# Performance work log

Measured on AMD Instinct MI355X. Metric: run time of the kernel, lower is better.

The kernel has to match this reference:

```python
import jax, jax.numpy as jnp
import numpy as np
import math

NUM_HEADS = 4
HIDDEN = 256
HEAD_DIM = HIDDEN // NUM_HEADS
NEG = jnp.finfo(jnp.float32).min


def setup_inputs() -> dict:
    key = jax.random.key(0)
    ks = jax.random.split(key, 8)
    B, Q, K = 4, 2048, 2048
    q_hidden_states = jax.random.normal(ks[0], (B, Q, HIDDEN), dtype=jnp.float32)
    k_hidden_states = jax.random.normal(ks[1], (B, K, HIDDEN), dtype=jnp.float32)
    attention_mask = jnp.zeros((B, 1, Q, K), dtype=jnp.float32)
    align_mask = jax.random.randint(ks[2], (B, K, Q), 0, 2, dtype=jnp.int32)
    s = 1.0 / math.sqrt(HIDDEN)
    Wq = jax.random.normal(ks[3], (HIDDEN, HIDDEN), dtype=jnp.float32) * s
    Wk = jax.random.normal(ks[4], (HIDDEN, HIDDEN), dtype=jnp.float32) * s
    Wv = jax.random.normal(ks[5], (HIDDEN, HIDDEN), dtype=jnp.float32) * s
    Wo = jax.random.normal(ks[6], (HIDDEN, HIDDEN), dtype=jnp.float32) * s
    return {"q_hidden_states": q_hidden_states, "k_hidden_states": k_hidden_states,
            "attention_mask": attention_mask, "align_mask": align_mask,
            "Wq": Wq, "Wk": Wk, "Wv": Wv, "Wo": Wo}


def reference(q_hidden_states, k_hidden_states, attention_mask, align_mask, Wq, Wk, Wv, Wo):
    B, Q, _ = q_hidden_states.shape
    K = k_hidden_states.shape[1]
    # torch Linear: y = x @ W.T  -> [B, S, H, D]
    q = (q_hidden_states @ Wq.T).reshape(B, Q, NUM_HEADS, HEAD_DIM)
    k = (k_hidden_states @ Wk.T).reshape(B, K, NUM_HEADS, HEAD_DIM)
    v = (k_hidden_states @ Wv.T).reshape(B, K, NUM_HEADS, HEAD_DIM)
    # scores: [B, H, Q, K]
    scores = jnp.einsum('bqhd,bkhd->bhqk', q, k) / math.sqrt(HEAD_DIM)
    # additive mask + clamp to finfo min
    scores = jnp.maximum(scores + attention_mask, NEG)
    # align_mask: (B, K, Q) -> (B, 1, Q, K); masked_fill where == 0
    am = jnp.transpose(align_mask, (0, 2, 1))[:, None, :, :]
    scores = jnp.where(am == 0, NEG, scores)
    scores = jnp.maximum(scores, NEG)
    probs = jax.nn.softmax(scores.astype(jnp.float32), axis=-1).astype(q.dtype)
    attn = jnp.einsum('bhqk,bkhd->bqhd', probs, v).reshape(B, Q, HIDDEN)
    return attn @ Wo.T
```

## Files before the change

### kernel.cpp

```cpp
#include <hip/hip_runtime.h>

#define NEGF -3.402823466e38f
#define MASKED_F -3.38953139e38f
#define LOG2E 1.44269504088896f
#define DEFER_THR 8.0f

typedef __attribute__((ext_vector_type(8))) short bf16x8;
typedef __attribute__((ext_vector_type(4))) float f32x4;
typedef __attribute__((ext_vector_type(4))) unsigned short u16x4;
typedef __attribute__((ext_vector_type(2))) unsigned int u32x2;

__device__ __forceinline__ unsigned short f2bf(float f) {
  unsigned u = __builtin_bit_cast(unsigned, f);
  u += 0x7fffu + ((u >> 16) & 1u);
  return (unsigned short)(u >> 16);
}

#define GLOAD_LDS16(gsrc, ldst)                                                     \
  __builtin_amdgcn_global_load_lds(                                                 \
      (const __attribute__((address_space(1))) void*)(gsrc),                        \
      (__attribute__((address_space(3))) void*)(ldst), 16, 0, 0)

#define OFF_QH  0u
#define OFF_KH  2097152u
#define OFF_W   4194304u
#define OFF_QP  4456448u
#define OFF_KP  6553600u
#define OFF_VT  8650752u
#define OFF_ATT 10747904u
#define OFF_M   12845056u
#define USHORT_USED 29622272u

__global__ __launch_bounds__(256) void k_convert(
    const float* __restrict__ qh, const float* __restrict__ kh,
    const float* __restrict__ w0, const float* __restrict__ w1,
    const float* __restrict__ w2, const float* __restrict__ w3,
    unsigned short* __restrict__ dst) {
  int v = blockIdx.x * 256 + threadIdx.x;
  const float* src;
  if (v < 524288)       src = qh + (size_t)v * 4;
  else if (v < 1048576) src = kh + ((size_t)v - 524288) * 4;
  else {
    int t = v - 1048576;
    int which = t >> 14;
    const float* w = (which == 0) ? w0 : (which == 1) ? w1 : (which == 2) ? w2 : w3;
    src = w + (size_t)(t & 16383) * 4;
  }
  f32x4 x = *(const f32x4*)src;
  u16x4 o;
  o[0] = f2bf(x[0]); o[1] = f2bf(x[1]); o[2] = f2bf(x[2]); o[3] = f2bf(x[3]);
  *(u16x4*)(dst + (size_t)v * 4) = o;
}

__global__ __launch_bounds__(256) void k_maskprep(const float* __restrict__ am,
    const int* __restrict__ al, unsigned short* __restrict__ M) {
  __shared__ float L[64 * 65];
  int bid = blockIdx.x;
  int b = bid >> 10, q64 = (bid >> 5) & 31, k64 = bid & 31;
  int t = threadIdx.x, c = t & 63, rg = t >> 6;

  const float* amb = am + ((size_t)b * 2048 + q64 * 64) * 2048 + k64 * 64;
#pragma unroll
  for (int i = 0; i < 16; ++i) {
    int row = i * 4 + rg;
    L[row * 65 + c] = amb[(size_t)row * 2048 + c] * LOG2E;
  }
  __syncthreads();
  const int* alb = al + ((size_t)b * 2048 + k64 * 64) * 2048 + q64 * 64;
#pragma unroll
  for (int i = 0; i < 16; ++i) {
    int kr = i * 4 + rg;
    if (alb[(size_t)kr * 2048 + c] == 0) L[c * 65 + kr] = MASKED_F;
  }
  __syncthreads();
  int w = t >> 6, lane = t & 63, l15 = lane & 15, l4 = lane >> 4;
  unsigned short* outp = M + ((((size_t)(b * 128 + q64 * 4 + w)) * 32 + k64) * 64 + lane) * 16;
#pragma unroll
  for (int kt = 0; kt < 4; ++kt) {
    u16x4 o;
#pragma unroll
    for (int r = 0; r < 4; ++r)
      o[r] = f2bf(L[(w * 16 + l15) * 65 + kt * 16 + l4 * 4 + r]);
    *(u16x4*)(outp + kt * 4) = o;
  }
}

__global__ __launch_bounds__(256) void k_proj(unsigned short* __restrict__ ws) {
  int bid = blockIdx.x;
  int mat = bid / 512;
  int rem = bid - mat * 512;
  int mt = rem >> 2, nt = rem & 3;
  int tid = threadIdx.x, w = tid >> 6, lane = tid & 63;
  int l15 = lane & 15, l4 = lane >> 4;

  const unsigned short* X = ws + (mat == 0 ? OFF_QH : OFF_KH);
  const unsigned short* W = ws + OFF_W + (size_t)mat * 65536;

  int i0 = mt * 64 + w * 16;
  int arow = i0 + l15;
  int koff = l4 * 8;

  f32x4 acc[4] = {};
  for (int ks = 0; ks < 8; ++ks) {
    bf16x8 a = *(const bf16x8*)(X + (size_t)arow * 256 + ks * 32 + koff);
#pragma unroll
    for (int ct = 0; ct < 4; ++ct) {
      bf16x8 bb = *(const bf16x8*)(W + (size_t)(nt * 64 + ct * 16 + l15) * 256 + ks * 32 + koff);
      acc[ct] = __builtin_amdgcn_mfma_f32_16x16x32_bf16(a, bb, acc[ct], 0, 0, 0);
    }
  }

  unsigned short* Qp = ws + OFF_QP;
  unsigned short* Kp = ws + OFF_KP;
  unsigned short* Vt = ws + OFF_VT;
  int rbase = i0 + l4 * 4;
#pragma unroll
  for (int ct = 0; ct < 4; ++ct) {
#pragma unroll
    for (int r = 0; r < 4; ++r) {
      int row = rbase + r;
      int b = row >> 11, s = row & 2047;
      int d = ct * 16 + l15;
      float v = acc[ct][r];
      if (mat == 0)      Qp[((size_t)(b * 4 + nt) * 2048 + s) * 64 + d] = f2bf(v * (0.125f * LOG2E));
      else if (mat == 1) Kp[((size_t)(b * 4 + nt) * 2048 + s) * 64 + d] = f2bf(v);
      else               Vt[((size_t)(b * 4 + nt) * 64 + d) * 2048 + s] = f2bf(v);
    }
  }
}

template <int NS>
__global__ __launch_bounds__(256) void k_attn(unsigned short* __restrict__ ws,
    float* __restrict__ po, float* __restrict__ pm, float* __restrict__ pl) {
  constexpr int LOG = (NS == 4) ? 2 : (NS == 2) ? 1 : 0;
  constexpr int SPAN = 2048 / NS;

  __shared__ __align__(16) unsigned short Kb[2][4096];
  __shared__ __align__(16) unsigned short Vb[2][4096];
  __shared__ __align__(16) unsigned short plds[4][1024];

  int bid = blockIdx.x;
  int sp = bid & (NS - 1);
  int qt = (bid >> LOG) & 31;
  int bh = bid >> (LOG + 5);
  int b = bh >> 2, h = bh & 3;
  int tid = threadIdx.x, w = tid >> 6, lane = tid & 63;
  int l15 = lane & 15, l4 = lane >> 4;
  int q0 = qt * 64 + w * 16;

  const unsigned short* Qp = ws + OFF_QP;
  const unsigned short* Kp = ws + OFF_KP + (size_t)bh * 2048 * 64;
  const unsigned short* Vt = ws + OFF_VT + (size_t)bh * 64 * 2048;
  const unsigned short* Mw = ws + OFF_M +
      (((size_t)(b * 128 + qt * 4 + w)) * 32) * 1024 + (size_t)lane * 16;

  int srow = lane >> 3;
  int scol = ((lane & 7) ^ srow) * 8;
  int c0 = w * 2;

  bf16x8 qf0 = *(const bf16x8*)(Qp + ((size_t)bh * 2048 + q0 + l15) * 64 + l4 * 8);
  bf16x8 qf1 = *(const bf16x8*)(Qp + ((size_t)bh * 2048 + q0 + l15) * 64 + 32 + l4 * 8);

  f32x4 o[4] = {};
  float mrun = -__builtin_inff();
  float lpart = 0.f;

  int kk0 = sp * SPAN;
#pragma unroll
  for (int c2 = 0; c2 < 2; ++c2) {
    int c = c0 + c2;
    GLOAD_LDS16(Kp + (size_t)(kk0 + c * 8 + srow) * 64 + scol, &Kb[0][c * 512]);
    GLOAD_LDS16(Vt + (size_t)(c * 8 + srow) * 2048 + kk0 + scol, &Vb[0][c * 512]);
  }
  __syncthreads();

  int cur = 0;
  for (int kk = kk0; kk < kk0 + SPAN; kk += 64) {
    if (kk + 64 < kk0 + SPAN) {
#pragma unroll
      for (int c2 = 0; c2 < 2; ++c2) {
        int c = c0 + c2;
        GLOAD_LDS16(Kp + (size_t)(kk + 64 + c * 8 + srow) * 64 + scol, &Kb[cur ^ 1][c * 512]);
        GLOAD_LDS16(Vt + (size_t)(c * 8 + srow) * 2048 + (kk + 64) + scol, &Vb[cur ^ 1][c * 512]);
      }
    }
    const unsigned short* mp = Mw + ((size_t)(kk >> 6)) * 1024;
    bf16x8 m0 = *(const bf16x8*)mp;
    bf16x8 m1 = *(const bf16x8*)(mp + 8);

    f32x4 sfr[4];
    __builtin_amdgcn_s_setprio(1);
#pragma unroll
    for (int kt = 0; kt < 4; ++kt) {
      int row = kt * 16 + l15;
      int sw = l15 & 7;
      bf16x8 k0 = *(const bf16x8*)&Kb[cur][row * 64 + ((l4 ^ sw) * 8)];
      bf16x8 k1 = *(const bf16x8*)&Kb[cur][row * 64 + (((4 + l4) ^ sw) * 8)];
      f32x4 acc = {};
      acc = __builtin_amdgcn_mfma_f32_16x16x32_bf16(k0, qf0, acc, 0, 0, 0);
      acc = __builtin_amdgcn_mfma_f32_16x16x32_bf16(k1, qf1, acc, 0, 0, 0);
      sfr[kt] = acc;
    }
    __builtin_amdgcn_s_setprio(0);

#pragma unroll
    for (int kt = 0; kt < 4; ++kt)
#pragma unroll
      for (int r = 0; r < 4; ++r) {
        int j = kt * 4 + r;
        unsigned short mu = (unsigned short)(j < 8 ? m0[j] : m1[j & 7]);
        sfr[kt][r] += __builtin_bit_cast(float, (unsigned)mu << 16);
      }

    float pmax = sfr[0][0];
#pragma unroll
    for (int kt = 0; kt < 4; ++kt)
#pragma unroll
      for (int r = 0; r < 4; ++r) pmax = fmaxf(pmax, sfr[kt][r]);
    pmax = fmaxf(pmax, __shfl_xor(pmax, 16));
    pmax = fmaxf(pmax, __shfl_xor(pmax, 32));

    if (__any(pmax > mrun + DEFER_THR)) {
      float mnew = fmaxf(mrun, pmax);
      float sfac = exp2f(mrun - mnew);
      mrun = mnew;
      lpart *= sfac;
#pragma unroll
      for (int r = 0; r < 4; ++r) {
        float sf = __shfl(sfac, l4 * 4 + r);
        o[0][r] *= sf; o[1][r] *= sf; o[2][r] *= sf; o[3][r] *= sf;
      }
    }

    float ls = 0.f;
#pragma unroll
    for (int kt = 0; kt < 4; ++kt)
#pragma unroll
      for (int r = 0; r < 4; ++r) {
        float e = exp2f(sfr[kt][r] - mrun);
        sfr[kt][r] = e;
        ls += e;
      }
    lpart += ls;

#pragma unroll
    for (int kt = 0; kt < 4; ++kt) {
      unsigned lo, hi;
      asm("v_cvt_pk_bf16_f32 %0, %1, %2" : "=v"(lo) : "v"(sfr[kt][0]), "v"(sfr[kt][1]));
      asm("v_cvt_pk_bf16_f32 %0, %1, %2" : "=v"(hi) : "v"(sfr[kt][2]), "v"(sfr[kt][3]));
      int chunk = kt * 2 + (l4 >> 1);
      int addr = l15 * 64 + (((chunk) ^ (l15 & 7)) << 3) + ((l4 & 1) << 2);
      u32x2 pk; pk[0] = lo; pk[1] = hi;
      *(u32x2*)&plds[w][addr] = pk;
    }

    __builtin_amdgcn_s_setprio(1);
#pragma unroll
    for (int ks = 0; ks < 2; ++ks) {
      int chnk = ks * 4 + l4;
      bf16x8 pa = *(const bf16x8*)&plds[w][l15 * 64 + ((chnk ^ (l15 & 7)) << 3)];
#pragma unroll
      for (int dt = 0; dt < 4; ++dt) {
        int row = dt * 16 + l15;
        bf16x8 vf = *(const bf16x8*)&Vb[cur][row * 64 + (((ks * 4 + l4) ^ (l15 & 7)) * 8)];
        o[dt] = __builtin_amdgcn_mfma_f32_16x16x32_bf16(pa, vf, o[dt], 0, 0, 0);
      }
    }
    __builtin_amdgcn_s_setprio(0);

    __syncthreads();
    cur ^= 1;
  }

  float lsum = lpart;
  lsum += __shfl_xor(lsum, 16);
  lsum += __shfl_xor(lsum, 32);

  if constexpr (NS == 1) {
    unsigned short* attnb = ws + OFF_ATT;
#pragma unroll
    for (int r = 0; r < 4; ++r) {
      float inv = 1.0f / __shfl(lsum, l4 * 4 + r);
      int qrow = q0 + l4 * 4 + r;
#pragma unroll
      for (int dt = 0; dt < 4; ++dt)
        attnb[(size_t)(b * 2048 + qrow) * 256 + h * 64 + dt * 16 + l15] = f2bf(o[dt][r] * inv);
    }
  } else {
    float* pob = po + (((size_t)sp * 16 + bh) * 2048) * 64;
#pragma unroll
    for (int r = 0; r < 4; ++r) {
      int qrow = q0 + l4 * 4 + r;
#pragma unroll
      for (int dt = 0; dt < 4; ++dt)
        pob[(size_t)qrow * 64 + dt * 16 + l15] = o[dt][r];
    }
    if (l4 == 0) {
      pm[(size_t)sp * 32768 + bh * 2048 + q0 + l15] = mrun;
      pl[(size_t)sp * 32768 + bh * 2048 + q0 + l15] = lsum;
    }
  }
}

template <int NS>
__global__ __launch_bounds__(256) void k_combine(const float* __restrict__ po,
    const float* __restrict__ pm, const float* __restrict__ pl,
    unsigned short* __restrict__ attnb) {
  int t = blockIdx.x * 256 + threadIdx.x;
  int d = t & 63;
  int row = t >> 6;

  float m[NS], l[NS];
  float M = -__builtin_inff();
#pragma unroll
  for (int sp = 0; sp < NS; ++sp) {
    m[sp] = pm[(size_t)sp * 32768 + row];
    l[sp] = pl[(size_t)sp * 32768 + row];
    M = fmaxf(M, m[sp]);
  }
  float denom = 0.f, acc = 0.f;
#pragma unroll
  for (int sp = 0; sp < NS; ++sp) {
    float wgt = exp2f(m[sp] - M);
    denom += l[sp] * wgt;
    acc += po[((size_t)sp * 32768 + row) * 64 + d] * wgt;
  }
  float val = acc / denom;
  int bh = row >> 11, qrow = row & 2047;
  int b = bh >> 2, h = bh & 3;
  attnb[((size_t)(b * 2048 + qrow)) * 256 + h * 64 + d] = f2bf(val);
}

__global__ __launch_bounds__(256) void k_oproj(const unsigned short* __restrict__ ws,
                                               float* __restrict__ out) {
  int bid = blockIdx.x;
  int mt = bid >> 2, nt = bid & 3;
  int tid = threadIdx.x, w = tid >> 6, lane = tid & 63;
  int l15 = lane & 15, l4 = lane >> 4;

  const unsigned short* A = ws + OFF_ATT;
  const unsigned short* W = ws + OFF_W + 3u * 65536u;
  int i0 = mt * 64 + w * 16;

  f32x4 acc[4] = {};
  for (int ks = 0; ks < 8; ++ks) {
    bf16x8 a = *(const bf16x8*)(A + (size_t)(i0 + l15) * 256 + ks * 32 + l4 * 8);
#pragma unroll
    for (int ct = 0; ct < 4; ++ct) {
      bf16x8 bb = *(const bf16x8*)(W + (size_t)(nt * 64 + ct * 16 + l15) * 256 + ks * 32 + l4 * 8);
      acc[ct] = __builtin_amdgcn_mfma_f32_16x16x32_bf16(a, bb, acc[ct], 0, 0, 0);
    }
  }
#pragma unroll
  for (int ct = 0; ct < 4; ++ct)
#pragma unroll
    for (int r = 0; r < 4; ++r)
      out[(size_t)(i0 + l4 * 4 + r) * 256 + nt * 64 + ct * 16 + l15] = acc[ct][r];
}

extern "C" void kernel_launch(void* const* d_in, const int* in_sizes, int n_in,
                              void* d_out, int out_size, void* d_ws, size_t ws_size,
                              hipStream_t stream) {
  const float* qh = (const float*)d_in[0];
  const float* kh = (const float*)d_in[1];
  const float* amask = (const float*)d_in[2];
  const int* alignm = (const int*)d_in[3];
  const float* Wq = (const float*)d_in[4];
  const float* Wk = (const float*)d_in[5];
  const float* Wv = (const float*)d_in[6];
  const float* Wo = (const float*)d_in[7];
  float* out = (float*)d_out;
  unsigned short* ws = (unsigned short*)d_ws;

  k_convert<<<4352, 256, 0, stream>>>(qh, kh, Wq, Wk, Wv, Wo, ws);
  k_maskprep<<<4096, 256, 0, stream>>>(amask, alignm, ws + OFF_M);
  k_proj<<<1536, 256, 0, stream>>>(ws);

  size_t avail_f = (ws_size > (size_t)USHORT_USED * 2)
                       ? (ws_size - (size_t)USHORT_USED * 2) / 4 : 0;
  auto need = [](int ns) { return (size_t)ns * (2097152 + 65536); };
  int NSv = (avail_f >= need(2)) ? 2 : 1;
  float* po = (float*)(ws + USHORT_USED);
  float* pm = po + (size_t)NSv * 2097152;
  float* pl = pm + (size_t)NSv * 32768;

  if (NSv == 2) {
    k_attn<2><<<1024, 256, 0, stream>>>(ws, po, pm, pl);
    k_combine<2><<<8192, 256, 0, stream>>>(po, pm, pl, ws + OFF_ATT);
  } else {
    k_attn<1><<<512, 256, 0, stream>>>(ws, po, pm, pl);
  }
  k_oproj<<<512, 256, 0, stream>>>(ws, out);
}
```

Baseline: 132.3 us.

## Replace bf16 combined mask prep with bit-packed align mask and direct fp32 additive mask reads

```diff
diff --git a/kernel.cpp b/kernel.cpp
--- a/kernel.cpp
+++ b/kernel.cpp
@@ -28,8 +28,8 @@
 #define OFF_KP  6553600u
 #define OFF_VT  8650752u
 #define OFF_ATT 10747904u
-#define OFF_M   12845056u
-#define USHORT_USED 29622272u
+#define OFF_BM  12845056u
+#define USHORT_USED 13893632u
 
 __global__ __launch_bounds__(256) void k_convert(
     const float* __restrict__ qh, const float* __restrict__ kh,
@@ -52,37 +52,18 @@
   *(u16x4*)(dst + (size_t)v * 4) = o;
 }
 
-__global__ __launch_bounds__(256) void k_maskprep(const float* __restrict__ am,
-    const int* __restrict__ al, unsigned short* __restrict__ M) {
-  __shared__ float L[64 * 65];
-  int bid = blockIdx.x;
-  int b = bid >> 10, q64 = (bid >> 5) & 31, k64 = bid & 31;
-  int t = threadIdx.x, c = t & 63, rg = t >> 6;
-
-  const float* amb = am + ((size_t)b * 2048 + q64 * 64) * 2048 + k64 * 64;
-#pragma unroll
-  for (int i = 0; i < 16; ++i) {
-    int row = i * 4 + rg;
-    L[row * 65 + c] = amb[(size_t)row * 2048 + c] * LOG2E;
-  }
-  __syncthreads();
-  const int* alb = al + ((size_t)b * 2048 + k64 * 64) * 2048 + q64 * 64;
-#pragma unroll
-  for (int i = 0; i < 16; ++i) {
-    int kr = i * 4 + rg;
-    if (alb[(size_t)kr * 2048 + c] == 0) L[c * 65 + kr] = MASKED_F;
-  }
-  __syncthreads();
-  int w = t >> 6, lane = t & 63, l15 = lane & 15, l4 = lane >> 4;
-  unsigned short* outp = M + ((((size_t)(b * 128 + q64 * 4 + w)) * 32 + k64) * 64 + lane) * 16;
-#pragma unroll
-  for (int kt = 0; kt < 4; ++kt) {
-    u16x4 o;
-#pragma unroll
-    for (int r = 0; r < 4; ++r)
-      o[r] = f2bf(L[(w * 16 + l15) * 65 + kt * 16 + l4 * 4 + r]);
-    *(u16x4*)(outp + kt * 4) = o;
-  }
+__global__ __launch_bounds__(256) void k_bitpack(const int* __restrict__ al,
+                                                 unsigned long long* __restrict__ bm) {
+  int wi = blockIdx.x * 256 + threadIdx.x;
+  int q = wi & 2047;
+  int k64 = (wi >> 11) & 31;
+  int b = wi >> 16;
+  const int* base = al + ((size_t)(b * 2048 + k64 * 64)) * 2048 + q;
+  unsigned long long word = 0;
+#pragma unroll
+  for (int k = 0; k < 64; ++k)
+    if (base[(size_t)k * 2048] != 0) word |= 1ull << k;
+  bm[wi] = word;
 }
 
 __global__ __launch_bounds__(256) void k_proj(unsigned short* __restrict__ ws) {
@@ -131,6 +112,7 @@
 
 template <int NS>
 __global__ __launch_bounds__(256) void k_attn(unsigned short* __restrict__ ws,
+    const float* __restrict__ am, const unsigned long long* __restrict__ bm,
     float* __restrict__ po, float* __restrict__ pm, float* __restrict__ pl) {
   constexpr int LOG = (NS == 4) ? 2 : (NS == 2) ? 1 : 0;
   constexpr int SPAN = 2048 / NS;
@@ -151,8 +133,8 @@
   const unsigned short* Qp = ws + OFF_QP;
   const unsigned short* Kp = ws + OFF_KP + (size_t)bh * 2048 * 64;
   const unsigned short* Vt = ws + OFF_VT + (size_t)bh * 64 * 2048;
-  const unsigned short* Mw = ws + OFF_M +
-      (((size_t)(b * 128 + qt * 4 + w)) * 32) * 1024 + (size_t)lane * 16;
+  const float* amq = am + ((size_t)(b * 2048 + q0 + l15)) * 2048;
+  const unsigned long long* bmq = bm + (size_t)b * 65536 + q0 + l15;
 
   int srow = lane >> 3;
   int scol = ((lane & 7) ^ srow) * 8;
@@ -164,6 +146,7 @@
   f32x4 o[4] = {};
   float mrun = -__builtin_inff();
   float lpart = 0.f;
+  int s0 = l4 * 4;
 
   int kk0 = sp * SPAN;
 #pragma unroll
@@ -184,9 +167,12 @@
         GLOAD_LDS16(Vt + (size_t)(c * 8 + srow) * 2048 + (kk + 64) + scol, &Vb[cur ^ 1][c * 512]);
       }
     }
-    const unsigned short* mp = Mw + ((size_t)(kk >> 6)) * 1024;
-    bf16x8 m0 = *(const bf16x8*)mp;
-    bf16x8 m1 = *(const bf16x8*)(mp + 8);
+    f32x4 a0 = *(const f32x4*)(amq + kk + 0 * 16 + s0);
+    f32x4 a1 = *(const f32x4*)(amq + kk + 1 * 16 + s0);
+    f32x4 a2 = *(const f32x4*)(amq + kk + 2 * 16 + s0);
+    f32x4 a3 = *(const f32x4*)(amq + kk + 3 * 16 + s0);
+    unsigned long long wbits = bmq[(size_t)(kk >> 6) * 2048];
+    unsigned blo = (unsigned)wbits, bhi = (unsigned)(wbits >> 32);
 
     f32x4 sfr[4];
     __builtin_amdgcn_s_setprio(1);
@@ -204,13 +190,16 @@
     __builtin_amdgcn_s_setprio(0);
 
 #pragma unroll
-    for (int kt = 0; kt < 4; ++kt)
+    for (int kt = 0; kt < 4; ++kt) {
+      unsigned half = (kt & 2) ? bhi : blo;
+      int base = (kt & 1) ? 16 + s0 : s0;
+      f32x4 a = (kt == 0) ? a0 : (kt == 1) ? a1 : (kt == 2) ? a2 : a3;
 #pragma unroll
       for (int r = 0; r < 4; ++r) {
-        int j = kt * 4 + r;
-        unsigned short mu = (unsigned short)(j < 8 ? m0[j] : m1[j & 7]);
-        sfr[kt][r] += __builtin_bit_cast(float, (unsigned)mu << 16);
-      }
+        float sc = fmaf(a[r], LOG2E, sfr[kt][r]);
+        sfr[kt][r] = ((half >> (base + r)) & 1u) ? sc : MASKED_F;
+      }
+    }
 
     float pmax = sfr[0][0];
 #pragma unroll
@@ -371,9 +360,10 @@
   const float* Wo = (const float*)d_in[7];
   float* out = (float*)d_out;
   unsigned short* ws = (unsigned short*)d_ws;
+  unsigned long long* bm = (unsigned long long*)(ws + OFF_BM);
 
   k_convert<<<4352, 256, 0, stream>>>(qh, kh, Wq, Wk, Wv, Wo, ws);
-  k_maskprep<<<4096, 256, 0, stream>>>(amask, alignm, ws + OFF_M);
+  k_bitpack<<<1024, 256, 0, stream>>>(alignm, bm);
   k_proj<<<1536, 256, 0, stream>>>(ws);
 
   size_t avail_f = (ws_size > (size_t)USHORT_USED * 2)
@@ -385,10 +375,10 @@
   float* pl = pm + (size_t)NSv * 32768;
 
   if (NSv == 2) {
-    k_attn<2><<<1024, 256, 0, stream>>>(ws, po, pm, pl);
+    k_attn<2><<<1024, 256, 0, stream>>>(ws, amask, bm, po, pm, pl);
     k_combine<2><<<8192, 256, 0, stream>>>(po, pm, pl, ws + OFF_ATT);
   } else {
-    k_attn<1><<<512, 256, 0, stream>>>(ws, po, pm, pl);
+    k_attn<1><<<512, 256, 0, stream>>>(ws, amask, bm, po, pm, pl);
   }
   k_oproj<<<512, 256, 0, stream>>>(ws, out);
 }
```

Result: slower. 140.4 us (+6.1%).
